# Performance work log

Measured on AMD Instinct MI355X. Metric: run time of the kernel, lower is better.

Reference implementation:

```python
import jax, jax.numpy as jnp
import numpy as np

HID = 128

def _lstm_layer(x, w_ih, w_hh, b_ih, b_hh):
    # x: [N, T, I]; PyTorch gate order: i, f, g, o
    n = x.shape[0]
    xg = jnp.einsum('nti,gi->ntg', x, w_ih) + b_ih + b_hh  # [N, T, 4H]
    xg = jnp.transpose(xg, (1, 0, 2))                       # [T, N, 4H]

    def step(carry, xg_t):
        h, c = carry
        g = xg_t + h @ w_hh.T                               # [N, 4H]
        i, f, gg, o = jnp.split(g, 4, axis=-1)
        i = jax.nn.sigmoid(i)
        f = jax.nn.sigmoid(f)
        gg = jnp.tanh(gg)
        o = jax.nn.sigmoid(o)
        c = f * c + i * gg
        h = o * jnp.tanh(c)
        return (h, c), h

    h0 = jnp.zeros((n, HID), dtype=x.dtype)
    c0 = jnp.zeros((n, HID), dtype=x.dtype)
    (hn, cn), hs = jax.lax.scan(step, (h0, c0), xg)
    return jnp.transpose(hs, (1, 0, 2))                     # [N, T, H]


def setup_inputs() -> dict:
    key = jax.random.key(0)
    ks = jax.random.split(key, 12)
    N = 8192
    s0 = 1.0 / np.sqrt(HID)
    u = lambda k, shape: jax.random.uniform(k, shape, jnp.float32, -s0, s0)
    return {
        'x': jax.random.normal(ks[0], (N, 1, 28, 28), jnp.float32),
        'w_ih0': u(ks[1], (4 * HID, 28)),
        'w_hh0': u(ks[2], (4 * HID, HID)),
        'b_ih0': u(ks[3], (4 * HID,)),
        'b_hh0': u(ks[4], (4 * HID,)),
        'w_ih1': u(ks[5], (4 * HID, HID)),
        'w_hh1': u(ks[6], (4 * HID, HID)),
        'b_ih1': u(ks[7], (4 * HID,)),
        'b_hh1': u(ks[8], (4 * HID,)),
        'w_out': u(ks[9], (10, HID)),
        'b_out': u(ks[10], (10,)),
    }


def reference(x, w_ih0, w_hh0, b_ih0, b_hh0, w_ih1, w_hh1, b_ih1, b_hh1, w_out, b_out):
    n, c, h, w = x.shape
    # permute(0,2,3,1).reshape(n, h, w*c) -> [N, 28, 28]
    seq = jnp.transpose(x, (0, 2, 3, 1)).reshape(n, h, w * c)
    hs1 = _lstm_layer(seq, w_ih0, w_hh0, b_ih0, b_hh0)
    hs2 = _lstm_layer(hs1, w_ih1, w_hh1, b_ih1, b_hh1)
    out = hs2[:, -1, :] @ w_out.T + b_out                   # [N, 10]
    return out
```

## Files before the change

kernel.cpp:

```cpp
#include <hip/hip_runtime.h>


typedef short  short8   __attribute__((ext_vector_type(8)));
typedef float  float4_t __attribute__((ext_vector_type(4)));

#define WIH1_OFF 0
#define H0_OFF   131072
#define H1_OFF   147456
#define X_OFF    155648
#define SMEM_SZ  157696

__device__ __forceinline__ unsigned short bf16r(float v) {
  union { float f; unsigned u; } x; x.f = v;
  unsigned r = x.u + 0x7fffu + ((x.u >> 16) & 1u);
  return (unsigned short)(r >> 16);
}
__device__ __forceinline__ float bf2f(unsigned short b) {
  union { unsigned u; float f; } x; x.u = ((unsigned)b) << 16;
  return x.f;
}
__device__ __forceinline__ float sigf(float x) {
  return __builtin_amdgcn_rcpf(1.0f + __expf(-x));
}
__device__ __forceinline__ float tanhfast(float x) {
  return 1.0f - 2.0f * __builtin_amdgcn_rcpf(__expf(2.0f * x) + 1.0f);
}

__global__ void pack_weights(const float* __restrict__ wih0, const float* __restrict__ whh0,
                             const float* __restrict__ wih1, const float* __restrict__ whh1,
                             unsigned short* __restrict__ dst)
{
  int e = blockIdx.x * 256 + threadIdx.x;
  const float* src; int K; int i;
  if      (e < 16384)  { src = wih0; K = 28;  i = e;          }
  else if (e < 81920)  { src = whh0; K = 128; i = e - 16384;  }
  else if (e < 147456) { src = wih1; K = 128; i = e - 81920;  }
  else if (e < 212992) { src = whh1; K = 128; i = e - 147456; }
  else return;
  int j = i & 7, lane = (i >> 3) & 63, tile = (i >> 9) & 31, kc = i >> 14;
  int row = tile * 16 + (lane & 15);
  int k = kc * 32 + ((lane >> 4) << 3) + j;
  float v = (k < K) ? src[row * K + k] : 0.0f;
  dst[e] = bf16r(v);
}

__global__ __launch_bounds__(512, 2)
void lstm_fused(const float* __restrict__ xg,
                const unsigned short* __restrict__ wpack,
                const float* __restrict__ bih0, const float* __restrict__ bhh0,
                const float* __restrict__ bih1, const float* __restrict__ bhh1,
                const float* __restrict__ wout, const float* __restrict__ bout,
                float* __restrict__ out)
{
  __shared__ __align__(16) char smem[SMEM_SZ];

  const int tid  = threadIdx.x;
  const int lane = tid & 63;
  const int wave = tid >> 6;
  const int q    = lane >> 4;
  const int mcol = lane & 15;
  const int n0   = blockIdx.x * 32;

  const short8* wp = (const short8*)wpack;

  short8 wih0[4], whh0[4][4], whh1[4][4];
#pragma unroll
  for (int g = 0; g < 4; ++g)
    wih0[g] = wp[(g * 8 + wave) * 64 + lane];
#pragma unroll
  for (int kc = 0; kc < 4; ++kc)
#pragma unroll
    for (int g = 0; g < 4; ++g) {
      whh0[kc][g] = wp[ 2048 + (kc * 32 + g * 8 + wave) * 64 + lane];
      whh1[kc][g] = wp[18432 + (kc * 32 + g * 8 + wave) * 64 + lane];
    }

  {
    short8* dstp = (short8*)smem;
#pragma unroll
    for (int rr = 0; rr < 16; ++rr)
      dstp[rr * 512 + tid] = wp[10240 + rr * 512 + tid];
  }

  float bias0[4], bias1[4];
  {
    const int d = wave * 16 + mcol;
#pragma unroll
    for (int g = 0; g < 4; ++g) {
      bias0[g] = bih0[g * 128 + d] + bhh0[g * 128 + d];
      bias1[g] = bih1[g * 128 + d] + bhh1[g * 128 + d];
    }
  }

  {
    int* z0 = (int*)(smem + H0_OFF + 8192);
    int* z1 = (int*)(smem + H1_OFF);
#pragma unroll
    for (int rr = 0; rr < 4; ++rr) { z0[rr * 512 + tid] = 0; z1[rr * 512 + tid] = 0; }
    ((int*)(smem + X_OFF))[tid] = 0;
  }

  auto stage_x = [&](int t) {
    if (tid < 448) {
      int s  = tid / 14;
      int kk = tid - s * 14;
      int k  = kk * 2;
      const float* xs = xg + (size_t)(n0 + s) * 784 + t * 28 + k;
      float v0 = xs[0], v1 = xs[1];
      unsigned u = (unsigned)bf16r(v0) | ((unsigned)bf16r(v1) << 16);
      int mt = s >> 4;
      int addr = X_OFF + mt * 1024 + ((((k >> 3) & 3) << 4) + (s & 15)) * 16 + (k & 7) * 2;
      *(unsigned*)(smem + addr) = u;
    }
  };
  stage_x(0);
  __syncthreads();

  const short8* Xf  = (const short8*)(smem + X_OFF);
  const short8* W1f = (const short8*)(smem + WIH1_OFF);
  const short8* H1f = (const short8*)(smem + H1_OFF);

  const int kc_d   = wave >> 1;
  const int sub    = ((wave & 1) << 1) | (mcol >> 3);
  const int hconst = kc_d * 1024 + sub * 256 + q * 64 + (mcol & 7) * 2;

  int h0r = H0_OFF + 8192, h0w = H0_OFF;

  float c0[2][4] = {{0.f,0.f,0.f,0.f},{0.f,0.f,0.f,0.f}};
  float c1[2][4] = {{0.f,0.f,0.f,0.f},{0.f,0.f,0.f,0.f}};

#pragma unroll 1
  for (int t = 0; t < 28; ++t) {
    float4_t acc[2][4];
    unsigned short hb[2][4];

#pragma unroll
    for (int mt = 0; mt < 2; ++mt)
#pragma unroll
      for (int g = 0; g < 4; ++g)
        acc[mt][g] = (float4_t){bias0[g], bias0[g], bias0[g], bias0[g]};
#pragma unroll
    for (int mt = 0; mt < 2; ++mt) {
      short8 xf = Xf[mt * 64 + lane];
#pragma unroll
      for (int g = 0; g < 4; ++g)
        acc[mt][g] = __builtin_amdgcn_mfma_f32_16x16x32_bf16(xf, wih0[g], acc[mt][g], 0, 0, 0);
    }
    {
      const short8* H0R = (const short8*)(smem + h0r);
#pragma unroll
      for (int kc = 0; kc < 4; ++kc)
#pragma unroll
        for (int mt = 0; mt < 2; ++mt) {
          short8 hf = H0R[(mt * 4 + kc) * 64 + lane];
#pragma unroll
          for (int g = 0; g < 4; ++g)
            acc[mt][g] = __builtin_amdgcn_mfma_f32_16x16x32_bf16(hf, whh0[kc][g], acc[mt][g], 0, 0, 0);
        }
    }
#pragma unroll
    for (int mt = 0; mt < 2; ++mt)
#pragma unroll
      for (int r = 0; r < 4; ++r) {
        float c = sigf(acc[mt][1][r]) * c0[mt][r] + sigf(acc[mt][0][r]) * tanhfast(acc[mt][2][r]);
        c0[mt][r] = c;
        *(unsigned short*)(smem + h0w + mt * 4096 + r * 16 + hconst) =
            bf16r(sigf(acc[mt][3][r]) * tanhfast(c));
      }

    __syncthreads();

    if (t < 27) stage_x(t + 1);

#pragma unroll
    for (int mt = 0; mt < 2; ++mt)
#pragma unroll
      for (int g = 0; g < 4; ++g)
        acc[mt][g] = (float4_t){bias1[g], bias1[g], bias1[g], bias1[g]};
    {
      const short8* H0W = (const short8*)(smem + h0w);
#pragma unroll
      for (int kc = 0; kc < 4; ++kc) {
        short8 wf[4];
#pragma unroll
        for (int g = 0; g < 4; ++g)
          wf[g] = W1f[(kc * 32 + g * 8 + wave) * 64 + lane];
#pragma unroll
        for (int mt = 0; mt < 2; ++mt) {
          short8 hf = H0W[(mt * 4 + kc) * 64 + lane];
#pragma unroll
          for (int g = 0; g < 4; ++g)
            acc[mt][g] = __builtin_amdgcn_mfma_f32_16x16x32_bf16(hf, wf[g], acc[mt][g], 0, 0, 0);
        }
      }
#pragma unroll
      for (int kc = 0; kc < 4; ++kc)
#pragma unroll
        for (int mt = 0; mt < 2; ++mt) {
          short8 hf = H1f[(mt * 4 + kc) * 64 + lane];
#pragma unroll
          for (int g = 0; g < 4; ++g)
            acc[mt][g] = __builtin_amdgcn_mfma_f32_16x16x32_bf16(hf, whh1[kc][g], acc[mt][g], 0, 0, 0);
        }
    }
#pragma unroll
    for (int mt = 0; mt < 2; ++mt)
#pragma unroll
      for (int r = 0; r < 4; ++r) {
        float c = sigf(acc[mt][1][r]) * c1[mt][r] + sigf(acc[mt][0][r]) * tanhfast(acc[mt][2][r]);
        c1[mt][r] = c;
        hb[mt][r] = bf16r(sigf(acc[mt][3][r]) * tanhfast(c));
      }

    __syncthreads();

#pragma unroll
    for (int mt = 0; mt < 2; ++mt)
#pragma unroll
      for (int r = 0; r < 4; ++r)
        *(unsigned short*)(smem + H1_OFF + mt * 4096 + r * 16 + hconst) = hb[mt][r];

    h0r ^= 8192; h0w ^= 8192;
  }
  __syncthreads();

  if (tid < 320) {
    int s = tid / 10, o = tid - (tid / 10) * 10;
    float sum = bout[o];
#pragma unroll
    for (int kc = 0; kc < 4; ++kc)
#pragma unroll
      for (int sb = 0; sb < 4; ++sb) {
        short8 hv = H1f[((s >> 4) * 4 + kc) * 64 + sb * 16 + (s & 15)];
        int dbase = kc * 32 + sb * 8;
        float4_t w0 = *(const float4_t*)(wout + o * 128 + dbase);
        float4_t w1 = *(const float4_t*)(wout + o * 128 + dbase + 4);
#pragma unroll
        for (int j = 0; j < 4; ++j) {
          sum += bf2f((unsigned short)hv[j])     * w0[j];
          sum += bf2f((unsigned short)hv[j + 4]) * w1[j];
        }
      }
    out[(size_t)(n0 + s) * 10 + o] = sum;
  }
}

extern "C" void kernel_launch(void* const* d_in, const int* in_sizes, int n_in,
                              void* d_out, int out_size, void* d_ws, size_t ws_size,
                              hipStream_t stream) {
  const float* x    = (const float*)d_in[0];
  const float* wih0 = (const float*)d_in[1];
  const float* whh0 = (const float*)d_in[2];
  const float* bih0 = (const float*)d_in[3];
  const float* bhh0 = (const float*)d_in[4];
  const float* wih1 = (const float*)d_in[5];
  const float* whh1 = (const float*)d_in[6];
  const float* bih1 = (const float*)d_in[7];
  const float* bhh1 = (const float*)d_in[8];
  const float* wout = (const float*)d_in[9];
  const float* bout = (const float*)d_in[10];

  unsigned short* wp = (unsigned short*)d_ws;

  pack_weights<<<832, 256, 0, stream>>>(wih0, whh0, wih1, whh1, wp);
  lstm_fused<<<256, 512, 0, stream>>>(x, wp, bih0, bhh0, bih1, bhh1, wout, bout,
                                      (float*)d_out);
}
```

Before: 219.0 us.

## Split LSTM block work across 16 waves, one M-tile per wave

Doubles the block to 1024 threads so each pair of waves shares a hidden-dimension slice and each wave handles one of the two 16-row batch tiles instead of both. This halves per-wave MFMA chains and accumulator registers on the serial recurrence, aiming for more latency hiding. In exchange every wave now holds its own register copy of the recurrent weights, and a larger block pays more for each barrier. Launch bounds of 1024 threads with 4 blocks requested is also unlikely to be achievable given the register-resident weights and about 154 KB of shared memory per block.

```diff
diff --git a/kernel.cpp b/kernel.cpp
--- a/kernel.cpp
+++ b/kernel.cpp
@@ -44,7 +44,7 @@
   dst[e] = bf16r(v);
 }
 
-__global__ __launch_bounds__(512, 2)
+__global__ __launch_bounds__(1024, 4)
 void lstm_fused(const float* __restrict__ xg,
                 const unsigned short* __restrict__ wpack,
                 const float* __restrict__ bih0, const float* __restrict__ bhh0,
@@ -54,37 +54,39 @@
 {
   __shared__ __align__(16) char smem[SMEM_SZ];
 
-  const int tid  = threadIdx.x;
-  const int lane = tid & 63;
-  const int wave = tid >> 6;
-  const int q    = lane >> 4;
-  const int mcol = lane & 15;
-  const int n0   = blockIdx.x * 32;
+  const int tid   = threadIdx.x;
+  const int lane  = tid & 63;
+  const int wave  = tid >> 6;
+  const int wavem = wave & 1;
+  const int waved = wave >> 1;
+  const int q     = lane >> 4;
+  const int mcol  = lane & 15;
+  const int n0    = blockIdx.x * 32;
 
   const short8* wp = (const short8*)wpack;
 
   short8 wih0[4], whh0[4][4], whh1[4][4];
 #pragma unroll
   for (int g = 0; g < 4; ++g)
-    wih0[g] = wp[(g * 8 + wave) * 64 + lane];
+    wih0[g] = wp[(g * 8 + waved) * 64 + lane];
 #pragma unroll
   for (int kc = 0; kc < 4; ++kc)
 #pragma unroll
     for (int g = 0; g < 4; ++g) {
-      whh0[kc][g] = wp[ 2048 + (kc * 32 + g * 8 + wave) * 64 + lane];
-      whh1[kc][g] = wp[18432 + (kc * 32 + g * 8 + wave) * 64 + lane];
+      whh0[kc][g] = wp[ 2048 + (kc * 32 + g * 8 + waved) * 64 + lane];
+      whh1[kc][g] = wp[18432 + (kc * 32 + g * 8 + waved) * 64 + lane];
     }
 
   {
     short8* dstp = (short8*)smem;
 #pragma unroll
-    for (int rr = 0; rr < 16; ++rr)
-      dstp[rr * 512 + tid] = wp[10240 + rr * 512 + tid];
+    for (int rr = 0; rr < 8; ++rr)
+      dstp[rr * 1024 + tid] = wp[10240 + rr * 1024 + tid];
   }
 
   float bias0[4], bias1[4];
   {
-    const int d = wave * 16 + mcol;
+    const int d = waved * 16 + mcol;
 #pragma unroll
     for (int g = 0; g < 4; ++g) {
       bias0[g] = bih0[g * 128 + d] + bhh0[g * 128 + d];
@@ -96,8 +98,8 @@
     int* z0 = (int*)(smem + H0_OFF + 8192);
     int* z1 = (int*)(smem + H1_OFF);
 #pragma unroll
-    for (int rr = 0; rr < 4; ++rr) { z0[rr * 512 + tid] = 0; z1[rr * 512 + tid] = 0; }
-    ((int*)(smem + X_OFF))[tid] = 0;
+    for (int rr = 0; rr < 2; ++rr) { z0[rr * 1024 + tid] = 0; z1[rr * 1024 + tid] = 0; }
+    if (tid < 512) ((int*)(smem + X_OFF))[tid] = 0;
   }
 
   auto stage_x = [&](int t) {
@@ -120,63 +122,54 @@
   const short8* W1f = (const short8*)(smem + WIH1_OFF);
   const short8* H1f = (const short8*)(smem + H1_OFF);
 
-  const int kc_d   = wave >> 1;
-  const int sub    = ((wave & 1) << 1) | (mcol >> 3);
+  const int kc_d   = waved >> 1;
+  const int sub    = ((waved & 1) << 1) | (mcol >> 3);
   const int hconst = kc_d * 1024 + sub * 256 + q * 64 + (mcol & 7) * 2;
 
   int h0r = H0_OFF + 8192, h0w = H0_OFF;
 
-  float c0[2][4] = {{0.f,0.f,0.f,0.f},{0.f,0.f,0.f,0.f}};
-  float c1[2][4] = {{0.f,0.f,0.f,0.f},{0.f,0.f,0.f,0.f}};
+  float c0[4] = {0.f, 0.f, 0.f, 0.f};
+  float c1[4] = {0.f, 0.f, 0.f, 0.f};
 
 #pragma unroll 1
   for (int t = 0; t < 28; ++t) {
-    float4_t acc[2][4];
-    unsigned short hb[2][4];
-
-#pragma unroll
-    for (int mt = 0; mt < 2; ++mt)
+    float4_t acc[4];
+    unsigned short hb[4];
+
+#pragma unroll
+    for (int g = 0; g < 4; ++g)
+      acc[g] = (float4_t){bias0[g], bias0[g], bias0[g], bias0[g]};
+    {
+      short8 xf = Xf[wavem * 64 + lane];
 #pragma unroll
       for (int g = 0; g < 4; ++g)
-        acc[mt][g] = (float4_t){bias0[g], bias0[g], bias0[g], bias0[g]};
-#pragma unroll
-    for (int mt = 0; mt < 2; ++mt) {
-      short8 xf = Xf[mt * 64 + lane];
-#pragma unroll
-      for (int g = 0; g < 4; ++g)
-        acc[mt][g] = __builtin_amdgcn_mfma_f32_16x16x32_bf16(xf, wih0[g], acc[mt][g], 0, 0, 0);
+        acc[g] = __builtin_amdgcn_mfma_f32_16x16x32_bf16(xf, wih0[g], acc[g], 0, 0, 0);
     }
     {
       const short8* H0R = (const short8*)(smem + h0r);
 #pragma unroll
-      for (int kc = 0; kc < 4; ++kc)
-#pragma unroll
-        for (int mt = 0; mt < 2; ++mt) {
-          short8 hf = H0R[(mt * 4 + kc) * 64 + lane];
-#pragma unroll
-          for (int g = 0; g < 4; ++g)
-            acc[mt][g] = __builtin_amdgcn_mfma_f32_16x16x32_bf16(hf, whh0[kc][g], acc[mt][g], 0, 0, 0);
-        }
-    }
-#pragma unroll
-    for (int mt = 0; mt < 2; ++mt)
-#pragma unroll
-      for (int r = 0; r < 4; ++r) {
-        float c = sigf(acc[mt][1][r]) * c0[mt][r] + sigf(acc[mt][0][r]) * tanhfast(acc[mt][2][r]);
-        c0[mt][r] = c;
-        *(unsigned short*)(smem + h0w + mt * 4096 + r * 16 + hconst) =
-            bf16r(sigf(acc[mt][3][r]) * tanhfast(c));
-      }
+      for (int kc = 0; kc < 4; ++kc) {
+        short8 hf = H0R[(wavem * 4 + kc) * 64 + lane];
+#pragma unroll
+        for (int g = 0; g < 4; ++g)
+          acc[g] = __builtin_amdgcn_mfma_f32_16x16x32_bf16(hf, whh0[kc][g], acc[g], 0, 0, 0);
+      }
+    }
+#pragma unroll
+    for (int r = 0; r < 4; ++r) {
+      float c = sigf(acc[1][r]) * c0[r] + sigf(acc[0][r]) * tanhfast(acc[2][r]);
+      c0[r] = c;
+      *(unsigned short*)(smem + h0w + wavem * 4096 + r * 16 + hconst) =
+          bf16r(sigf(acc[3][r]) * tanhfast(c));
+    }
 
     __syncthreads();
 
     if (t < 27) stage_x(t + 1);
 
 #pragma unroll
-    for (int mt = 0; mt < 2; ++mt)
-#pragma unroll
-      for (int g = 0; g < 4; ++g)
-        acc[mt][g] = (float4_t){bias1[g], bias1[g], bias1[g], bias1[g]};
+    for (int g = 0; g < 4; ++g)
+      acc[g] = (float4_t){bias1[g], bias1[g], bias1[g], bias1[g]};
     {
       const short8* H0W = (const short8*)(smem + h0w);
 #pragma unroll
@@ -184,41 +177,32 @@
         short8 wf[4];
 #pragma unroll
         for (int g = 0; g < 4; ++g)
-          wf[g] = W1f[(kc * 32 + g * 8 + wave) * 64 + lane];
-#pragma unroll
-        for (int mt = 0; mt < 2; ++mt) {
-          short8 hf = H0W[(mt * 4 + kc) * 64 + lane];
-#pragma unroll
-          for (int g = 0; g < 4; ++g)
-            acc[mt][g] = __builtin_amdgcn_mfma_f32_16x16x32_bf16(hf, wf[g], acc[mt][g], 0, 0, 0);
-        }
-      }
-#pragma unroll
-      for (int kc = 0; kc < 4; ++kc)
-#pragma unroll
-        for (int mt = 0; mt < 2; ++mt) {
-          short8 hf = H1f[(mt * 4 + kc) * 64 + lane];
-#pragma unroll
-          for (int g = 0; g < 4; ++g)
-            acc[mt][g] = __builtin_amdgcn_mfma_f32_16x16x32_bf16(hf, whh1[kc][g], acc[mt][g], 0, 0, 0);
-        }
-    }
-#pragma unroll
-    for (int mt = 0; mt < 2; ++mt)
-#pragma unroll
-      for (int r = 0; r < 4; ++r) {
-        float c = sigf(acc[mt][1][r]) * c1[mt][r] + sigf(acc[mt][0][r]) * tanhfast(acc[mt][2][r]);
-        c1[mt][r] = c;
-        hb[mt][r] = bf16r(sigf(acc[mt][3][r]) * tanhfast(c));
-      }
+          wf[g] = W1f[(kc * 32 + g * 8 + waved) * 64 + lane];
+        short8 hf = H0W[(wavem * 4 + kc) * 64 + lane];
+#pragma unroll
+        for (int g = 0; g < 4; ++g)
+          acc[g] = __builtin_amdgcn_mfma_f32_16x16x32_bf16(hf, wf[g], acc[g], 0, 0, 0);
+      }
+#pragma unroll
+      for (int kc = 0; kc < 4; ++kc) {
+        short8 hf = H1f[(wavem * 4 + kc) * 64 + lane];
+#pragma unroll
+        for (int g = 0; g < 4; ++g)
+          acc[g] = __builtin_amdgcn_mfma_f32_16x16x32_bf16(hf, whh1[kc][g], acc[g], 0, 0, 0);
+      }
+    }
+#pragma unroll
+    for (int r = 0; r < 4; ++r) {
+      float c = sigf(acc[1][r]) * c1[r] + sigf(acc[0][r]) * tanhfast(acc[2][r]);
+      c1[r] = c;
+      hb[r] = bf16r(sigf(acc[3][r]) * tanhfast(c));
+    }
 
     __syncthreads();
 
 #pragma unroll
-    for (int mt = 0; mt < 2; ++mt)
-#pragma unroll
-      for (int r = 0; r < 4; ++r)
-        *(unsigned short*)(smem + H1_OFF + mt * 4096 + r * 16 + hconst) = hb[mt][r];
+    for (int r = 0; r < 4; ++r)
+      *(unsigned short*)(smem + H1_OFF + wavem * 4096 + r * 16 + hconst) = hb[r];
 
     h0r ^= 8192; h0w ^= 8192;
   }
@@ -263,6 +247,6 @@
   unsigned short* wp = (unsigned short*)d_ws;
 
   pack_weights<<<832, 256, 0, stream>>>(wih0, whh0, wih1, whh1, wp);
-  lstm_fused<<<256, 512, 0, stream>>>(x, wp, bih0, bhh0, bih1, bhh1, wout, bout,
-                                      (float*)d_out);
-}
+  lstm_fused<<<256, 1024, 0, stream>>>(x, wp, bih0, bhh0, bih1, bhh1, wout, bout,
+                                       (float*)d_out);
+}
```

After: 524.4 us. 2.39x slower.
